# Kernel optimization log

Hardware: AMD Instinct MI355X
Metric: run time of the kernel (lower is better)

Reference implementation:

```python
import jax, jax.numpy as jnp
import numpy as np

N, T, VN, C = 64, 512, 10, 128
HEADS, DH = 8, 16
INNER = HEADS * DH  # 128
BN_EPS = 1e-5


def _build_mask():
    # depth == 0 graph: facial-region connections + self links, symmetric 10x10
    m = np.zeros((VN, VN), dtype=np.float32)
    conn = [[0, 1], [0, 2], [2, 1], [3, 4], [3, 5], [4, 5],
            [6, 7], [6, 8], [6, 9], [8, 7], [9, 7], [8, 9]]
    for a, b in conn:
        m[a, b] = 1.0
        m[b, a] = 1.0
    for i in range(VN):
        m[i, i] = 1.0
    return jnp.asarray(m)


def setup_inputs() -> dict:
    key = jax.random.key(0)
    k = jax.random.split(key, 6)
    x = jax.random.normal(k[0], (N, T, VN, C), dtype=jnp.float32)
    gamma = 1.0 + 0.02 * jax.random.normal(k[1], (C,), dtype=jnp.float32)
    beta = 0.02 * jax.random.normal(k[2], (C,), dtype=jnp.float32)
    w_qkv = 0.02 * jax.random.normal(k[3], (C, 3 * INNER), dtype=jnp.float32)
    w_out = 0.02 * jax.random.normal(k[4], (INNER, C), dtype=jnp.float32)
    b_out = 0.02 * jax.random.normal(k[5], (C,), dtype=jnp.float32)
    return {"x": x, "gamma": gamma, "beta": beta, "w_qkv": w_qkv,
            "w_out": w_out, "b_out": b_out, "mask": _build_mask()}


def reference(x, gamma, beta, w_qkv, w_out, b_out, mask):
    n, t, vn, c = x.shape
    xb = x.reshape(-1, vn, c)                     # (b, vn, c), b = n*t
    # BatchNorm1d over channel c (training mode: batch stats over b and vn)
    mean = jnp.mean(xb, axis=(0, 1))
    var = jnp.var(xb, axis=(0, 1))                # biased, matches torch BN
    y = (xb - mean) * jax.lax.rsqrt(var + BN_EPS) * gamma + beta
    # fused QKV projection (Linear, no bias)
    qkv = y @ w_qkv                               # (b, vn, 3*inner)
    q, k, v = jnp.split(qkv, 3, axis=-1)
    split_heads = lambda z: z.reshape(-1, vn, HEADS, DH).transpose(0, 2, 1, 3)
    q, k, v = split_heads(q), split_heads(k), split_heads(v)  # (b, h, vn, dh)
    scale = DH ** -0.5
    dots = jnp.einsum('bhid,bhjd->bhij', q, k) * scale
    dots = dots * mask                            # multiplicative graph mask
    attn = jax.nn.softmax(dots, axis=-1)
    out = jnp.einsum('bhij,bhjd->bhid', attn, v)  # (b, h, vn, dh)
    out = out.transpose(0, 2, 1, 3).reshape(-1, vn, INNER)
    out = out @ w_out + b_out                     # output projection
    return out.reshape(n, t, vn, c)
```

## Files before the change

### kernel.cpp

```cpp
#include <hip/hip_runtime.h>


#define VNODES 10
#define CH 128
#define ROWS_TOTAL 327680
#define G 4
#define MROWS 40
#define MT 3
#define SX 136
#define SK 132

typedef __bf16 bf16x8 __attribute__((ext_vector_type(8)));
typedef __bf16 bf16x2 __attribute__((ext_vector_type(2)));
typedef float f32x4 __attribute__((ext_vector_type(4)));
typedef float f32x2 __attribute__((ext_vector_type(2)));
typedef unsigned u32x4 __attribute__((ext_vector_type(4)));
typedef unsigned u32x2 __attribute__((ext_vector_type(2)));

__device__ __forceinline__ unsigned short f2bfu(float f) {
    __bf16 h = (__bf16)f;
    return __builtin_bit_cast(unsigned short, h);
}
__device__ __forceinline__ unsigned packcvt(float a, float b) {
    bf16x2 t;
    t[0] = (__bf16)a;
    t[1] = (__bf16)b;
    return __builtin_bit_cast(unsigned, t);
}
__device__ __forceinline__ f32x2 up2(unsigned u) {
    f32x2 r;
    r[0] = __uint_as_float(u << 16);
    r[1] = __uint_as_float(u & 0xffff0000u);
    return r;
}

__global__ __launch_bounds__(256) void stats_kernel(
        const float* __restrict__ x,
        float* __restrict__ ws_sum, float* __restrict__ ws_sq) {
    __shared__ float lsum[8][128];
    __shared__ float lsq[8][128];
    int t = threadIdx.x;
    int slot = t >> 5, g = t & 31;
    float s[4], q[4];
#pragma unroll
    for (int k = 0; k < 4; ++k) { s[k] = 0.f; q[k] = 0.f; }
    size_t base_row = (size_t)blockIdx.x * 160;
    for (int p = 0; p < 20; ++p) {
        size_t row = base_row + p * 8 + slot;
        f32x4 v = *(const f32x4*)(x + row * CH + g * 4);
#pragma unroll
        for (int k = 0; k < 4; ++k) {
            s[k] += v[k];
            q[k] = fmaf(v[k], v[k], q[k]);
        }
    }
#pragma unroll
    for (int k = 0; k < 4; ++k) { lsum[slot][g * 4 + k] = s[k]; lsq[slot][g * 4 + k] = q[k]; }
    __syncthreads();
    if (t < 128) {
        float ts = 0.f, tq = 0.f;
#pragma unroll
        for (int sl = 0; sl < 8; ++sl) { ts += lsum[sl][t]; tq += lsq[sl][t]; }
        atomicAdd(&ws_sum[t], ts);
        atomicAdd(&ws_sq[t], tq);
    }
}

__global__ __launch_bounds__(256) void prep_kernel(
        const float* __restrict__ wqkv, const float* __restrict__ wout,
        const float* __restrict__ gamma, const float* __restrict__ beta,
        const float* __restrict__ stats,
        unsigned short* __restrict__ fq, unsigned short* __restrict__ fo,
        float* __restrict__ bq) {
    __shared__ float sh_s[128];
    if (blockIdx.x < 32) {
        int tid = blockIdx.x * 256 + threadIdx.x;
        if (tid < 24 * 4 * 64) {
            int l = tid & 63;
            int kt = (tid >> 6) & 3;
            int nt = tid >> 8;
            int quad = l >> 4, n = l & 15;
#pragma unroll
            for (int j = 0; j < 8; ++j) {
                int k = kt * 32 + quad * 8 + j;
                float mean = stats[k] * (1.0f / ROWS_TOTAL);
                float var = stats[128 + k] * (1.0f / ROWS_TOTAL) - mean * mean;
                float sc = gamma[k] * rsqrtf(var + 1e-5f);
                fq[tid * 8 + j] = f2bfu(sc * wqkv[k * 384 + nt * 16 + n]);
            }
        } else if (tid < 24 * 4 * 64 + 8 * 4 * 64) {
            int u = tid - 24 * 4 * 64;
            int l = u & 63;
            int kt = (u >> 6) & 3;
            int nt = u >> 8;
            int quad = l >> 4, n = l & 15;
#pragma unroll
            for (int j = 0; j < 8; ++j) {
                int k = kt * 32 + quad * 8 + j;
                fo[u * 8 + j] = f2bfu(wout[k * 128 + nt * 16 + n]);
            }
        }
    } else {
        int t = threadIdx.x;
        if (t < 128) {
            float mean = stats[t] * (1.0f / ROWS_TOTAL);
            float var = stats[128 + t] * (1.0f / ROWS_TOTAL) - mean * mean;
            float sc = gamma[t] * rsqrtf(var + 1e-5f);
            sh_s[t] = beta[t] - mean * sc;
        }
        __syncthreads();
        for (int n = t; n < 384; n += 256) {
            float acc = 0.f;
#pragma unroll 8
            for (int c = 0; c < 128; ++c) acc = fmaf(sh_s[c], wqkv[c * 384 + n], acc);
            bq[n] = acc;
        }
    }
}

__global__ __launch_bounds__(512, 6) void main_kernel(
        const float* __restrict__ x,
        const float* __restrict__ maskp,
        const float* __restrict__ bq,
        const unsigned short* __restrict__ wqkv_f,
        const unsigned short* __restrict__ wout_f,
        const float* __restrict__ b_out,
        float* __restrict__ out) {
    __shared__ __align__(16) unsigned short xT[48 * SX];
    __shared__ __align__(16) unsigned short qT[40 * SX];
    __shared__ __align__(16) unsigned short kvT[80 * SX];
    __shared__ float bq_s[384], bout_s[128], mask_s[VNODES * VNODES];

    unsigned short* kTb = kvT;
    unsigned short* vTb = kvT + 40 * SX;
    float* oT = (float*)kvT;

    int tid = threadIdx.x;
    int lane = tid & 63, w = tid >> 6;
    size_t row0 = (size_t)blockIdx.x * MROWS;

    if (tid < 384) bq_s[tid] = bq[tid];
    else bout_s[tid - 384] = b_out[tid - 384];
    if (tid < VNODES * VNODES) mask_s[tid] = maskp[tid];
    {
        int r = 40 + (tid >> 6), c = (tid & 63) * 2;
        *(unsigned*)(xT + r * SX + c) = 0u;
    }

    {
#pragma unroll
        for (int p = 0; p < 3; ++p) {
            int idx = p * 512 + tid;
            if (idx < 1280) {
                int r = idx >> 5, g = idx & 31;
                f32x4 v = *(const f32x4*)(x + (row0 + r) * CH + g * 4);
                u32x2 two;
                two[0] = packcvt(v[0], v[1]);
                two[1] = packcvt(v[2], v[3]);
                *(u32x2*)(xT + r * SX + g * 4) = two;
            }
        }
    }
    __syncthreads();

    {
        bf16x8 bf[3][4];
#pragma unroll
        for (int ni = 0; ni < 3; ++ni) {
            int nt = w + ni * 8;
#pragma unroll
            for (int kt = 0; kt < 4; ++kt)
                bf[ni][kt] = *(const bf16x8*)(wqkv_f + ((nt * 4 + kt) * 64 + lane) * 8);
        }
        int l15 = lane & 15, quad = lane >> 4;
        for (int mt = 0; mt < MT; ++mt) {
            bf16x8 a[4];
#pragma unroll
            for (int kt = 0; kt < 4; ++kt)
                a[kt] = *(const bf16x8*)(xT + (mt * 16 + l15) * SX + kt * 32 + quad * 8);
            f32x4 accq = {0.f,0.f,0.f,0.f}, acck = {0.f,0.f,0.f,0.f}, accv = {0.f,0.f,0.f,0.f};
#pragma unroll
            for (int kt = 0; kt < 4; ++kt) {
                accq = __builtin_amdgcn_mfma_f32_16x16x32_bf16(a[kt], bf[0][kt], accq, 0, 0, 0);
                acck = __builtin_amdgcn_mfma_f32_16x16x32_bf16(a[kt], bf[1][kt], acck, 0, 0, 0);
                accv = __builtin_amdgcn_mfma_f32_16x16x32_bf16(a[kt], bf[2][kt], accv, 0, 0, 0);
            }
            int col = w * 16 + l15;
            float bqq = bq_s[col], bqk = bq_s[128 + col], bqv = bq_s[256 + col];
#pragma unroll
            for (int i = 0; i < 4; ++i) {
                int rr = mt * 16 + quad * 4 + i;
                if (rr < MROWS) {
                    qT[rr * SX + col]  = f2bfu((accq[i] + bqq) * 0.25f);
                    kTb[rr * SX + col] = f2bfu(acck[i] + bqk);
                    vTb[rr * SX + col] = f2bfu(accv[i] + bqv);
                }
            }
        }
    }
    __syncthreads();

    if (tid < G * 8 * VNODES) {
        int h = tid / (G * VNODES);
        int rem = tid - h * (G * VNODES);
        int b = rem / VNODES;
        int i = rem - b * VNODES;
        int rowi = b * VNODES + i;
        const unsigned* qp = (const unsigned*)(qT + rowi * SX + h * 16);
        u32x4 qw0 = *(const u32x4*)qp;
        u32x4 qw1 = *(const u32x4*)(qp + 4);
        f32x2 qv[8];
#pragma unroll
        for (int d = 0; d < 4; ++d) {
            qv[d]     = up2(qw0[d]);
            qv[4 + d] = up2(qw1[d]);
        }
        float p[VNODES];
        float mx = -1e30f;
#pragma unroll
        for (int j = 0; j < VNODES; ++j) {
            const unsigned* kp = (const unsigned*)(kTb + (b * VNODES + j) * SX + h * 16);
            u32x4 k0 = *(const u32x4*)kp;
            u32x4 k1 = *(const u32x4*)(kp + 4);
            f32x2 acc2 = {0.f, 0.f};
#pragma unroll
            for (int d = 0; d < 4; ++d) {
                acc2 = __builtin_elementwise_fma(qv[d],     up2(k0[d]), acc2);
                acc2 = __builtin_elementwise_fma(qv[4 + d], up2(k1[d]), acc2);
            }
            p[j] = (acc2[0] + acc2[1]) * mask_s[i * VNODES + j];
            mx = fmaxf(mx, p[j]);
        }
        float s = 0.f;
#pragma unroll
        for (int j = 0; j < VNODES; ++j) { p[j] = __expf(p[j] - mx); s += p[j]; }
        float inv = 1.0f / s;
        f32x2 o2[8];
#pragma unroll
        for (int d = 0; d < 8; ++d) o2[d] = (f32x2){0.f, 0.f};
#pragma unroll
        for (int j = 0; j < VNODES; ++j) {
            const unsigned* vp = (const unsigned*)(vTb + (b * VNODES + j) * SX + h * 16);
            u32x4 v0 = *(const u32x4*)vp;
            u32x4 v1 = *(const u32x4*)(vp + 4);
            f32x2 pp = {p[j], p[j]};
#pragma unroll
            for (int d = 0; d < 4; ++d) {
                o2[d]     = __builtin_elementwise_fma(pp, up2(v0[d]), o2[d]);
                o2[4 + d] = __builtin_elementwise_fma(pp, up2(v1[d]), o2[4 + d]);
            }
        }
        f32x2 iv = {inv, inv};
#pragma unroll
        for (int d2 = 0; d2 < 8; ++d2) {
            f32x2 r = o2[d2] * iv;
            *(unsigned*)(xT + rowi * SX + h * 16 + d2 * 2) = packcvt(r[0], r[1]);
        }
    }
    __syncthreads();

    {
        bf16x8 bfw[4];
#pragma unroll
        for (int kt = 0; kt < 4; ++kt)
            bfw[kt] = *(const bf16x8*)(wout_f + ((w * 4 + kt) * 64 + lane) * 8);
        int l15 = lane & 15, quad = lane >> 4;
        int col = w * 16 + l15;
        float bias = bout_s[col];
        for (int mt = 0; mt < MT; ++mt) {
            f32x4 acc = {0.f, 0.f, 0.f, 0.f};
#pragma unroll
            for (int kt = 0; kt < 4; ++kt) {
                bf16x8 a = *(const bf16x8*)(xT + (mt * 16 + l15) * SX + kt * 32 + quad * 8);
                acc = __builtin_amdgcn_mfma_f32_16x16x32_bf16(a, bfw[kt], acc, 0, 0, 0);
            }
#pragma unroll
            for (int i = 0; i < 4; ++i) {
                int rr = mt * 16 + quad * 4 + i;
                if (rr < MROWS) oT[rr * SK + col] = acc[i] + bias;
            }
        }
    }
    __syncthreads();

    {
#pragma unroll
        for (int p = 0; p < 3; ++p) {
            int idx = p * 512 + tid;
            if (idx < 1280) {
                int r = idx >> 5, g = idx & 31;
                *(f32x4*)(out + (row0 + r) * CH + g * 4) = *(const f32x4*)(oT + r * SK + g * 4);
            }
        }
    }
}

extern "C" void kernel_launch(void* const* d_in, const int* in_sizes, int n_in,
                              void* d_out, int out_size, void* d_ws, size_t ws_size,
                              hipStream_t stream) {
    const float* x     = (const float*)d_in[0];
    const float* gamma = (const float*)d_in[1];
    const float* beta  = (const float*)d_in[2];
    const float* wqkv  = (const float*)d_in[3];
    const float* wout  = (const float*)d_in[4];
    const float* bout  = (const float*)d_in[5];
    const float* maskp = (const float*)d_in[6];
    float* out = (float*)d_out;

    char* ws = (char*)d_ws;
    float* ws_stats = (float*)ws;
    float* bq = (float*)(ws + 1024);
    unsigned short* fq = (unsigned short*)(ws + 4096);
    unsigned short* fo = (unsigned short*)(ws + 4096 + 98304);

    hipMemsetAsync(ws, 0, 1024, stream);
    stats_kernel<<<2048, 256, 0, stream>>>(x, ws_stats, ws_stats + 128);
    prep_kernel<<<33, 256, 0, stream>>>(wqkv, wout, gamma, beta, ws_stats, fq, fo, bq);
    main_kernel<<<8192, 512, 0, stream>>>(x, maskp, bq, fq, fo, bout, out);
}
```

Measured before the change: 443.9 us.

## Make main kernel persistent with register prefetch of next chunk

The main kernel becomes persistent: 512 blocks loop over 8192 chunks of 40 rows. Weight fragments and biases are loaded once per block, and the next chunk's x tile is prefetched into registers while the current chunk is computed. Output is written straight from the MFMA accumulators with nontemporal scalar stores, which drops the LDS staging buffer and one barrier. The costs are lower occupancy (launch bounds go from 6 to 4 waves), more register pressure, and scattered 4-byte output stores in place of 16-byte vector stores.

```diff
diff --git a/kernel.cpp b/kernel.cpp
--- a/kernel.cpp
+++ b/kernel.cpp
@@ -8,7 +8,8 @@
 #define MROWS 40
 #define MT 3
 #define SX 136
-#define SK 132
+#define NCHUNK 8192
+#define GRID 512
 
 typedef __bf16 bf16x8 __attribute__((ext_vector_type(8)));
 typedef __bf16 bf16x2 __attribute__((ext_vector_type(2)));
@@ -118,7 +119,7 @@
     }
 }
 
-__global__ __launch_bounds__(512, 6) void main_kernel(
+__global__ __launch_bounds__(512, 4) void main_kernel(
         const float* __restrict__ x,
         const float* __restrict__ maskp,
         const float* __restrict__ bq,
@@ -128,16 +129,14 @@
         float* __restrict__ out) {
     __shared__ __align__(16) unsigned short xT[48 * SX];
     __shared__ __align__(16) unsigned short qT[40 * SX];
-    __shared__ __align__(16) unsigned short kvT[80 * SX];
+    __shared__ __align__(16) unsigned short kTb[40 * SX];
+    __shared__ __align__(16) unsigned short vTb[40 * SX];
     __shared__ float bq_s[384], bout_s[128], mask_s[VNODES * VNODES];
-
-    unsigned short* kTb = kvT;
-    unsigned short* vTb = kvT + 40 * SX;
-    float* oT = (float*)kvT;
 
     int tid = threadIdx.x;
     int lane = tid & 63, w = tid >> 6;
-    size_t row0 = (size_t)blockIdx.x * MROWS;
+    int l15 = lane & 15, quad = lane >> 4;
+    int col = w * 16 + l15;
 
     if (tid < 384) bq_s[tid] = bq[tid];
     else bout_s[tid - 384] = b_out[tid - 384];
@@ -147,151 +146,162 @@
         *(unsigned*)(xT + r * SX + c) = 0u;
     }
 
+    bf16x8 wq[3][4];
+#pragma unroll
+    for (int ni = 0; ni < 3; ++ni)
+#pragma unroll
+        for (int kt = 0; kt < 4; ++kt)
+            wq[ni][kt] = *(const bf16x8*)(wqkv_f + (((w + ni * 8) * 4 + kt) * 64 + lane) * 8);
+    bf16x8 wo[4];
+#pragma unroll
+    for (int kt = 0; kt < 4; ++kt)
+        wo[kt] = *(const bf16x8*)(wout_f + ((w * 4 + kt) * 64 + lane) * 8);
+
+    __syncthreads();
+    float bqq4 = bq_s[col] * 0.25f;
+    float bqk = bq_s[128 + col], bqv = bq_s[256 + col];
+    float bias = bout_s[col];
+
+    int c = blockIdx.x;
+    f32x4 pf0, pf1, pf2;
     {
-#pragma unroll
-        for (int p = 0; p < 3; ++p) {
-            int idx = p * 512 + tid;
-            if (idx < 1280) {
-                int r = idx >> 5, g = idx & 31;
-                f32x4 v = *(const f32x4*)(x + (row0 + r) * CH + g * 4);
-                u32x2 two;
-                two[0] = packcvt(v[0], v[1]);
-                two[1] = packcvt(v[2], v[3]);
-                *(u32x2*)(xT + r * SX + g * 4) = two;
-            }
-        }
-    }
-    __syncthreads();
-
-    {
-        bf16x8 bf[3][4];
-#pragma unroll
-        for (int ni = 0; ni < 3; ++ni) {
-            int nt = w + ni * 8;
-#pragma unroll
-            for (int kt = 0; kt < 4; ++kt)
-                bf[ni][kt] = *(const bf16x8*)(wqkv_f + ((nt * 4 + kt) * 64 + lane) * 8);
-        }
-        int l15 = lane & 15, quad = lane >> 4;
-        for (int mt = 0; mt < MT; ++mt) {
-            bf16x8 a[4];
-#pragma unroll
-            for (int kt = 0; kt < 4; ++kt)
-                a[kt] = *(const bf16x8*)(xT + (mt * 16 + l15) * SX + kt * 32 + quad * 8);
-            f32x4 accq = {0.f,0.f,0.f,0.f}, acck = {0.f,0.f,0.f,0.f}, accv = {0.f,0.f,0.f,0.f};
-#pragma unroll
-            for (int kt = 0; kt < 4; ++kt) {
-                accq = __builtin_amdgcn_mfma_f32_16x16x32_bf16(a[kt], bf[0][kt], accq, 0, 0, 0);
-                acck = __builtin_amdgcn_mfma_f32_16x16x32_bf16(a[kt], bf[1][kt], acck, 0, 0, 0);
-                accv = __builtin_amdgcn_mfma_f32_16x16x32_bf16(a[kt], bf[2][kt], accv, 0, 0, 0);
-            }
-            int col = w * 16 + l15;
-            float bqq = bq_s[col], bqk = bq_s[128 + col], bqv = bq_s[256 + col];
-#pragma unroll
-            for (int i = 0; i < 4; ++i) {
-                int rr = mt * 16 + quad * 4 + i;
-                if (rr < MROWS) {
-                    qT[rr * SX + col]  = f2bfu((accq[i] + bqq) * 0.25f);
-                    kTb[rr * SX + col] = f2bfu(acck[i] + bqk);
-                    vTb[rr * SX + col] = f2bfu(accv[i] + bqv);
-                }
-            }
-        }
-    }
-    __syncthreads();
-
-    if (tid < G * 8 * VNODES) {
-        int h = tid / (G * VNODES);
-        int rem = tid - h * (G * VNODES);
-        int b = rem / VNODES;
-        int i = rem - b * VNODES;
-        int rowi = b * VNODES + i;
-        const unsigned* qp = (const unsigned*)(qT + rowi * SX + h * 16);
-        u32x4 qw0 = *(const u32x4*)qp;
-        u32x4 qw1 = *(const u32x4*)(qp + 4);
-        f32x2 qv[8];
-#pragma unroll
-        for (int d = 0; d < 4; ++d) {
-            qv[d]     = up2(qw0[d]);
-            qv[4 + d] = up2(qw1[d]);
-        }
-        float p[VNODES];
-        float mx = -1e30f;
-#pragma unroll
-        for (int j = 0; j < VNODES; ++j) {
-            const unsigned* kp = (const unsigned*)(kTb + (b * VNODES + j) * SX + h * 16);
-            u32x4 k0 = *(const u32x4*)kp;
-            u32x4 k1 = *(const u32x4*)(kp + 4);
-            f32x2 acc2 = {0.f, 0.f};
+        const float* xb = x + (size_t)c * (MROWS * CH);
+        pf0 = *(const f32x4*)(xb + tid * 4);
+        pf1 = *(const f32x4*)(xb + 2048 + tid * 4);
+        if (tid < 256) pf2 = *(const f32x4*)(xb + 4096 + tid * 4);
+    }
+
+    while (true) {
+        size_t row0 = (size_t)c * MROWS;
+
+        {
+            int r = tid >> 5, g = tid & 31;
+            u32x2 t0; t0[0] = packcvt(pf0[0], pf0[1]); t0[1] = packcvt(pf0[2], pf0[3]);
+            *(u32x2*)(xT + r * SX + g * 4) = t0;
+            u32x2 t1; t1[0] = packcvt(pf1[0], pf1[1]); t1[1] = packcvt(pf1[2], pf1[3]);
+            *(u32x2*)(xT + (r + 16) * SX + g * 4) = t1;
+            if (tid < 256) {
+                u32x2 t2; t2[0] = packcvt(pf2[0], pf2[1]); t2[1] = packcvt(pf2[2], pf2[3]);
+                *(u32x2*)(xT + (r + 32) * SX + g * 4) = t2;
+            }
+        }
+        __syncthreads();
+
+        int cn = c + GRID;
+        bool more = cn < NCHUNK;
+        if (more) {
+            const float* xb = x + (size_t)cn * (MROWS * CH);
+            pf0 = *(const f32x4*)(xb + tid * 4);
+            pf1 = *(const f32x4*)(xb + 2048 + tid * 4);
+            if (tid < 256) pf2 = *(const f32x4*)(xb + 4096 + tid * 4);
+        }
+
+        {
+            for (int mt = 0; mt < MT; ++mt) {
+                bf16x8 a[4];
+#pragma unroll
+                for (int kt = 0; kt < 4; ++kt)
+                    a[kt] = *(const bf16x8*)(xT + (mt * 16 + l15) * SX + kt * 32 + quad * 8);
+                f32x4 accq = {0.f,0.f,0.f,0.f}, acck = {0.f,0.f,0.f,0.f}, accv = {0.f,0.f,0.f,0.f};
+#pragma unroll
+                for (int kt = 0; kt < 4; ++kt) {
+                    accq = __builtin_amdgcn_mfma_f32_16x16x32_bf16(a[kt], wq[0][kt], accq, 0, 0, 0);
+                    acck = __builtin_amdgcn_mfma_f32_16x16x32_bf16(a[kt], wq[1][kt], acck, 0, 0, 0);
+                    accv = __builtin_amdgcn_mfma_f32_16x16x32_bf16(a[kt], wq[2][kt], accv, 0, 0, 0);
+                }
+#pragma unroll
+                for (int i = 0; i < 4; ++i) {
+                    int rr = mt * 16 + quad * 4 + i;
+                    if (rr < MROWS) {
+                        qT[rr * SX + col]  = f2bfu(fmaf(accq[i], 0.25f, bqq4));
+                        kTb[rr * SX + col] = f2bfu(acck[i] + bqk);
+                        vTb[rr * SX + col] = f2bfu(accv[i] + bqv);
+                    }
+                }
+            }
+        }
+        __syncthreads();
+
+        if (tid < G * 8 * VNODES) {
+            int h = tid / (G * VNODES);
+            int rem = tid - h * (G * VNODES);
+            int b = rem / VNODES;
+            int i = rem - b * VNODES;
+            int rowi = b * VNODES + i;
+            const unsigned* qp = (const unsigned*)(qT + rowi * SX + h * 16);
+            u32x4 qw0 = *(const u32x4*)qp;
+            u32x4 qw1 = *(const u32x4*)(qp + 4);
+            f32x2 qv[8];
 #pragma unroll
             for (int d = 0; d < 4; ++d) {
-                acc2 = __builtin_elementwise_fma(qv[d],     up2(k0[d]), acc2);
-                acc2 = __builtin_elementwise_fma(qv[4 + d], up2(k1[d]), acc2);
-            }
-            p[j] = (acc2[0] + acc2[1]) * mask_s[i * VNODES + j];
-            mx = fmaxf(mx, p[j]);
-        }
-        float s = 0.f;
-#pragma unroll
-        for (int j = 0; j < VNODES; ++j) { p[j] = __expf(p[j] - mx); s += p[j]; }
-        float inv = 1.0f / s;
-        f32x2 o2[8];
-#pragma unroll
-        for (int d = 0; d < 8; ++d) o2[d] = (f32x2){0.f, 0.f};
-#pragma unroll
-        for (int j = 0; j < VNODES; ++j) {
-            const unsigned* vp = (const unsigned*)(vTb + (b * VNODES + j) * SX + h * 16);
-            u32x4 v0 = *(const u32x4*)vp;
-            u32x4 v1 = *(const u32x4*)(vp + 4);
-            f32x2 pp = {p[j], p[j]};
-#pragma unroll
-            for (int d = 0; d < 4; ++d) {
-                o2[d]     = __builtin_elementwise_fma(pp, up2(v0[d]), o2[d]);
-                o2[4 + d] = __builtin_elementwise_fma(pp, up2(v1[d]), o2[4 + d]);
-            }
-        }
-        f32x2 iv = {inv, inv};
-#pragma unroll
-        for (int d2 = 0; d2 < 8; ++d2) {
-            f32x2 r = o2[d2] * iv;
-            *(unsigned*)(xT + rowi * SX + h * 16 + d2 * 2) = packcvt(r[0], r[1]);
-        }
-    }
-    __syncthreads();
-
-    {
-        bf16x8 bfw[4];
-#pragma unroll
-        for (int kt = 0; kt < 4; ++kt)
-            bfw[kt] = *(const bf16x8*)(wout_f + ((w * 4 + kt) * 64 + lane) * 8);
-        int l15 = lane & 15, quad = lane >> 4;
-        int col = w * 16 + l15;
-        float bias = bout_s[col];
-        for (int mt = 0; mt < MT; ++mt) {
-            f32x4 acc = {0.f, 0.f, 0.f, 0.f};
-#pragma unroll
-            for (int kt = 0; kt < 4; ++kt) {
-                bf16x8 a = *(const bf16x8*)(xT + (mt * 16 + l15) * SX + kt * 32 + quad * 8);
-                acc = __builtin_amdgcn_mfma_f32_16x16x32_bf16(a, bfw[kt], acc, 0, 0, 0);
-            }
-#pragma unroll
-            for (int i = 0; i < 4; ++i) {
-                int rr = mt * 16 + quad * 4 + i;
-                if (rr < MROWS) oT[rr * SK + col] = acc[i] + bias;
-            }
-        }
-    }
-    __syncthreads();
-
-    {
-#pragma unroll
-        for (int p = 0; p < 3; ++p) {
-            int idx = p * 512 + tid;
-            if (idx < 1280) {
-                int r = idx >> 5, g = idx & 31;
-                *(f32x4*)(out + (row0 + r) * CH + g * 4) = *(const f32x4*)(oT + r * SK + g * 4);
-            }
-        }
+                qv[d]     = up2(qw0[d]);
+                qv[4 + d] = up2(qw1[d]);
+            }
+            float p[VNODES];
+            float mx = -1e30f;
+#pragma unroll
+            for (int j = 0; j < VNODES; ++j) {
+                const unsigned* kp = (const unsigned*)(kTb + (b * VNODES + j) * SX + h * 16);
+                u32x4 k0 = *(const u32x4*)kp;
+                u32x4 k1 = *(const u32x4*)(kp + 4);
+                f32x2 acc2 = {0.f, 0.f};
+#pragma unroll
+                for (int d = 0; d < 4; ++d) {
+                    acc2 = __builtin_elementwise_fma(qv[d],     up2(k0[d]), acc2);
+                    acc2 = __builtin_elementwise_fma(qv[4 + d], up2(k1[d]), acc2);
+                }
+                p[j] = (acc2[0] + acc2[1]) * mask_s[i * VNODES + j];
+                mx = fmaxf(mx, p[j]);
+            }
+            float s = 0.f;
+#pragma unroll
+            for (int j = 0; j < VNODES; ++j) { p[j] = __expf(p[j] - mx); s += p[j]; }
+            float inv = 1.0f / s;
+            f32x2 o2[8];
+#pragma unroll
+            for (int d = 0; d < 8; ++d) o2[d] = (f32x2){0.f, 0.f};
+#pragma unroll
+            for (int j = 0; j < VNODES; ++j) {
+                const unsigned* vp = (const unsigned*)(vTb + (b * VNODES + j) * SX + h * 16);
+                u32x4 v0 = *(const u32x4*)vp;
+                u32x4 v1 = *(const u32x4*)(vp + 4);
+                f32x2 pp = {p[j], p[j]};
+#pragma unroll
+                for (int d = 0; d < 4; ++d) {
+                    o2[d]     = __builtin_elementwise_fma(pp, up2(v0[d]), o2[d]);
+                    o2[4 + d] = __builtin_elementwise_fma(pp, up2(v1[d]), o2[4 + d]);
+                }
+            }
+            f32x2 iv = {inv, inv};
+#pragma unroll
+            for (int d2 = 0; d2 < 8; ++d2) {
+                f32x2 r = o2[d2] * iv;
+                *(unsigned*)(xT + rowi * SX + h * 16 + d2 * 2) = packcvt(r[0], r[1]);
+            }
+        }
+        __syncthreads();
+
+        {
+            for (int mt = 0; mt < MT; ++mt) {
+                f32x4 acc = {0.f, 0.f, 0.f, 0.f};
+#pragma unroll
+                for (int kt = 0; kt < 4; ++kt) {
+                    bf16x8 a = *(const bf16x8*)(xT + (mt * 16 + l15) * SX + kt * 32 + quad * 8);
+                    acc = __builtin_amdgcn_mfma_f32_16x16x32_bf16(a, wo[kt], acc, 0, 0, 0);
+                }
+#pragma unroll
+                for (int i = 0; i < 4; ++i) {
+                    int rr = mt * 16 + quad * 4 + i;
+                    if (rr < MROWS)
+                        __builtin_nontemporal_store(acc[i] + bias,
+                                                    out + (row0 + rr) * CH + col);
+                }
+            }
+        }
+
+        if (!more) break;
+        __syncthreads();
+        c = cn;
     }
 }
 
@@ -316,5 +326,5 @@
     hipMemsetAsync(ws, 0, 1024, stream);
     stats_kernel<<<2048, 256, 0, stream>>>(x, ws_stats, ws_stats + 128);
     prep_kernel<<<33, 256, 0, stream>>>(wqkv, wout, gamma, beta, ws_stats, fq, fo, bq);
-    main_kernel<<<8192, 512, 0, stream>>>(x, maskp, bq, fq, fo, bout, out);
-}
+    main_kernel<<<GRID, 512, 0, stream>>>(x, maskp, bq, fq, fo, bout, out);
+}
```

Result: slower. 491.6 us (+10.7%).

## Spread BN stat atomics over replicas and write output directly from MFMA

Applied to the files above, without the earlier changes.

The stats kernel now spreads its atomic adds over 32 replicated accumulator slots instead of one, which should reduce contention on the 256 stat addresses. The prep kernel sums the replicas into shared memory before using them. The main kernel drops the LDS staging of the output tile and the extra barrier, and gives K and V their own buffers instead of aliasing them. MFMA results are now stored straight to global memory with per-element stores, which are less coalesced and raise LDS use slightly, possibly lowering occupancy.

```diff
diff --git a/kernel.cpp b/kernel.cpp
--- a/kernel.cpp
+++ b/kernel.cpp
@@ -8,7 +8,7 @@
 #define MROWS 40
 #define MT 3
 #define SX 136
-#define SK 132
+#define REP 32
 
 typedef __bf16 bf16x8 __attribute__((ext_vector_type(8)));
 typedef __bf16 bf16x2 __attribute__((ext_vector_type(2)));
@@ -36,7 +36,7 @@
 
 __global__ __launch_bounds__(256) void stats_kernel(
         const float* __restrict__ x,
-        float* __restrict__ ws_sum, float* __restrict__ ws_sq) {
+        float* __restrict__ ws_rep) {
     __shared__ float lsum[8][128];
     __shared__ float lsq[8][128];
     int t = threadIdx.x;
@@ -61,18 +61,29 @@
         float ts = 0.f, tq = 0.f;
 #pragma unroll
         for (int sl = 0; sl < 8; ++sl) { ts += lsum[sl][t]; tq += lsq[sl][t]; }
-        atomicAdd(&ws_sum[t], ts);
-        atomicAdd(&ws_sq[t], tq);
+        float* rep = ws_rep + (blockIdx.x & (REP - 1)) * 256;
+        atomicAdd(&rep[t], ts);
+        atomicAdd(&rep[128 + t], tq);
     }
 }
 
 __global__ __launch_bounds__(256) void prep_kernel(
         const float* __restrict__ wqkv, const float* __restrict__ wout,
         const float* __restrict__ gamma, const float* __restrict__ beta,
-        const float* __restrict__ stats,
+        const float* __restrict__ ws_rep,
         unsigned short* __restrict__ fq, unsigned short* __restrict__ fo,
         float* __restrict__ bq) {
+    __shared__ float sh_stats[256];
     __shared__ float sh_s[128];
+    {
+        int t = threadIdx.x;
+        float acc = 0.f;
+#pragma unroll
+        for (int r = 0; r < REP; ++r) acc += ws_rep[r * 256 + t];
+        sh_stats[t] = acc;
+    }
+    __syncthreads();
+
     if (blockIdx.x < 32) {
         int tid = blockIdx.x * 256 + threadIdx.x;
         if (tid < 24 * 4 * 64) {
@@ -83,8 +94,8 @@
 #pragma unroll
             for (int j = 0; j < 8; ++j) {
                 int k = kt * 32 + quad * 8 + j;
-                float mean = stats[k] * (1.0f / ROWS_TOTAL);
-                float var = stats[128 + k] * (1.0f / ROWS_TOTAL) - mean * mean;
+                float mean = sh_stats[k] * (1.0f / ROWS_TOTAL);
+                float var = sh_stats[128 + k] * (1.0f / ROWS_TOTAL) - mean * mean;
                 float sc = gamma[k] * rsqrtf(var + 1e-5f);
                 fq[tid * 8 + j] = f2bfu(sc * wqkv[k * 384 + nt * 16 + n]);
             }
@@ -103,8 +114,8 @@
     } else {
         int t = threadIdx.x;
         if (t < 128) {
-            float mean = stats[t] * (1.0f / ROWS_TOTAL);
-            float var = stats[128 + t] * (1.0f / ROWS_TOTAL) - mean * mean;
+            float mean = sh_stats[t] * (1.0f / ROWS_TOTAL);
+            float var = sh_stats[128 + t] * (1.0f / ROWS_TOTAL) - mean * mean;
             float sc = gamma[t] * rsqrtf(var + 1e-5f);
             sh_s[t] = beta[t] - mean * sc;
         }
@@ -128,12 +139,9 @@
         float* __restrict__ out) {
     __shared__ __align__(16) unsigned short xT[48 * SX];
     __shared__ __align__(16) unsigned short qT[40 * SX];
-    __shared__ __align__(16) unsigned short kvT[80 * SX];
+    __shared__ __align__(16) unsigned short kTb[40 * SX];
+    __shared__ __align__(16) unsigned short vTb[40 * SX];
     __shared__ float bq_s[384], bout_s[128], mask_s[VNODES * VNODES];
-
-    unsigned short* kTb = kvT;
-    unsigned short* vTb = kvT + 40 * SX;
-    float* oT = (float*)kvT;
 
     int tid = threadIdx.x;
     int lane = tid & 63, w = tid >> 6;
@@ -277,19 +285,7 @@
 #pragma unroll
             for (int i = 0; i < 4; ++i) {
                 int rr = mt * 16 + quad * 4 + i;
-                if (rr < MROWS) oT[rr * SK + col] = acc[i] + bias;
-            }
-        }
-    }
-    __syncthreads();
-
-    {
-#pragma unroll
-        for (int p = 0; p < 3; ++p) {
-            int idx = p * 512 + tid;
-            if (idx < 1280) {
-                int r = idx >> 5, g = idx & 31;
-                *(f32x4*)(out + (row0 + r) * CH + g * 4) = *(const f32x4*)(oT + r * SK + g * 4);
+                if (rr < MROWS) out[(row0 + rr) * CH + col] = acc[i] + bias;
             }
         }
     }
@@ -308,13 +304,13 @@
     float* out = (float*)d_out;
 
     char* ws = (char*)d_ws;
-    float* ws_stats = (float*)ws;
-    float* bq = (float*)(ws + 1024);
-    unsigned short* fq = (unsigned short*)(ws + 4096);
-    unsigned short* fo = (unsigned short*)(ws + 4096 + 98304);
-
-    hipMemsetAsync(ws, 0, 1024, stream);
-    stats_kernel<<<2048, 256, 0, stream>>>(x, ws_stats, ws_stats + 128);
-    prep_kernel<<<33, 256, 0, stream>>>(wqkv, wout, gamma, beta, ws_stats, fq, fo, bq);
+    float* ws_rep = (float*)ws;
+    float* bq = (float*)(ws + REP * 1024);
+    unsigned short* fq = (unsigned short*)(ws + REP * 1024 + 4096);
+    unsigned short* fo = (unsigned short*)(ws + REP * 1024 + 4096 + 98304);
+
+    hipMemsetAsync(ws, 0, REP * 1024, stream);
+    stats_kernel<<<2048, 256, 0, stream>>>(x, ws_rep);
+    prep_kernel<<<33, 256, 0, stream>>>(wqkv, wout, gamma, beta, ws_rep, fq, fo, bq);
     main_kernel<<<8192, 512, 0, stream>>>(x, maskp, bq, fq, fo, bout, out);
 }
```

Result: faster. 402.1 us (-9.4%).
